# Kernel tuning notes

Measured on AMD Instinct MI355X. Metric: run time of the kernel, lower is better.

Reference implementation:

```python
import jax, jax.numpy as jnp
import numpy as np
from jax import lax

B, T, C_IN, HID, K, HORIZON = 64, 1024, 256, 512, 3, 12
OUT_DIM = HORIZON * 3


def causal_conv(x, w, b, dilation):
    # x: (B, C_in, T), w: (C_out, C_in, K) -> left-padded causal conv == conv+Chomp1d
    pad = (K - 1) * dilation
    y = lax.conv_general_dilated(x, w, window_strides=(1,), padding=[(pad, 0)],
                                 rhs_dilation=(dilation,),
                                 dimension_numbers=('NCH', 'OIH', 'NCH'))
    return y + b[None, :, None]


def setup_inputs() -> dict:
    key = jax.random.key(0)
    ks = jax.random.split(key, 16)
    N = B * T
    x = jax.random.normal(ks[0], (N, C_IN), jnp.float32)
    edge_index = jax.random.randint(ks[1], (2, N), 0, N, dtype=jnp.int64)
    idx = jnp.arange(N, dtype=jnp.int64)
    batch = idx // T          # graph id per node
    node_time = idx % T       # local time per node
    s1 = 1.0 / np.sqrt(C_IN * K)
    s2 = 1.0 / np.sqrt(HID * K)
    sd = 1.0 / np.sqrt(C_IN)
    sf = 1.0 / np.sqrt(HID)
    return {
        'x': x, 'edge_index': edge_index, 'batch': batch, 'node_time': node_time,
        # TemporalBlock 0 (in=C_IN, out=HID, dilation=1)
        'conv1_w0': jax.random.uniform(ks[2], (HID, C_IN, K), jnp.float32, -s1, s1),
        'conv1_b0': jax.random.uniform(ks[3], (HID,), jnp.float32, -s1, s1),
        'conv2_w0': jax.random.uniform(ks[4], (HID, HID, K), jnp.float32, -s2, s2),
        'conv2_b0': jax.random.uniform(ks[5], (HID,), jnp.float32, -s2, s2),
        'down_w0': jax.random.uniform(ks[6], (HID, C_IN, 1), jnp.float32, -sd, sd),
        'down_b0': jax.random.uniform(ks[7], (HID,), jnp.float32, -sd, sd),
        # TemporalBlock 1 (in=HID, out=HID, dilation=2, no downsample)
        'conv1_w1': jax.random.uniform(ks[8], (HID, HID, K), jnp.float32, -s2, s2),
        'conv1_b1': jax.random.uniform(ks[9], (HID,), jnp.float32, -s2, s2),
        'conv2_w1': jax.random.uniform(ks[10], (HID, HID, K), jnp.float32, -s2, s2),
        'conv2_b1': jax.random.uniform(ks[11], (HID,), jnp.float32, -s2, s2),
        # fc
        'fc_w': jax.random.uniform(ks[12], (OUT_DIM, HID), jnp.float32, -sf, sf),
        'fc_b': jax.random.uniform(ks[13], (OUT_DIM,), jnp.float32, -sf, sf),
    }


def reference(x, edge_index, batch, node_time,
              conv1_w0, conv1_b0, conv2_w0, conv2_b0, down_w0, down_b0,
              conv1_w1, conv1_b1, conv2_w1, conv2_b1, fc_w, fc_b):
    # vectorized scatter replacing the per-node Python loop
    x_seq = jnp.zeros((B, T, C_IN), x.dtype).at[batch, node_time].set(x)
    h = x_seq.transpose(0, 2, 1)  # (B, C_IN, T)
    # TemporalBlock 0 (dropout inactive in eval)
    out = jax.nn.relu(causal_conv(h, conv1_w0, conv1_b0, 1))
    out = jax.nn.relu(causal_conv(out, conv2_w0, conv2_b0, 1))
    res = jnp.einsum('bct,oc->bot', h, down_w0[:, :, 0]) + down_b0[None, :, None]
    h = jax.nn.relu(out + res)
    # TemporalBlock 1
    out = jax.nn.relu(causal_conv(h, conv1_w1, conv1_b1, 2))
    out = jax.nn.relu(causal_conv(out, conv2_w1, conv2_b1, 2))
    h = jax.nn.relu(out + h)
    # last timestep -> fc
    return h[:, :, -1] @ fc_w.T + fc_b
```

## Files before the change

### kernel.cpp

```cpp
#include <hip/hip_runtime.h>


#define OUTD 36

template <int CIN, int TS_N, int TP, int TOUT, int S, int D, int OFF, int TAPS,
          int OCT, int CCH, int NCH, bool SRC_X, int TS_BASE, int TS_STEP>
__device__ __forceinline__ void conv_body(int bx, int by,
                                          const float* __restrict__ src,
                                          const float* __restrict__ w,
                                          float* __restrict__ Pout) {
    const int tid = threadIdx.x, lane = tid & 63, wv = tid >> 6;
    const int oc0 = bx * OCT;
    constexpr int OCR = OCT / 4;
    __shared__ float Als[CCH * TAPS * OCT];
    __shared__ float Bls[CCH * 64 * TP];
    float acc[OCR][TOUT];
#pragma unroll
    for (int i = 0; i < OCR; ++i)
#pragma unroll
        for (int t = 0; t < TOUT; ++t) acc[i][t] = 0.f;

    for (int ch = 0; ch < NCH; ++ch) {
        const int c0 = (by * NCH + ch) * CCH;
        if (ch) __syncthreads();
        for (int idx = tid; idx < OCT * CCH * TAPS; idx += 256) {
            int i = idx / (CCH * TAPS), r = idx % (CCH * TAPS);
            int c = r / TAPS, kk = r % TAPS;
            Als[(c * TAPS + kk) * OCT + i] =
                w[(size_t)(oc0 + i) * (CIN * TAPS) + (c0 + c) * TAPS + kk];
        }
        if constexpr (SRC_X) {
            for (int idx = tid; idx < CCH * TS_N * 64; idx += 256) {
                int c = idx % CCH, rb = idx / CCH;
                int b = rb & 63, u = rb >> 6;
                Bls[(c * 64 + b) * TP + u] =
                    src[((size_t)b * 1024 + 1011 + TS_BASE + TS_STEP * u) * 256 +
                        c0 + c];
            }
        } else {
            const float4* gp = (const float4*)(src + (size_t)c0 * 64 * TP);
            float4* lp = (float4*)Bls;
            for (int idx = tid; idx < CCH * 64 * TP / 4; idx += 256)
                lp[idx] = gp[idx];
        }
        __syncthreads();
        constexpr int NLOAD = (TP % 4 == 0) ? TP : TS_N;
        for (int c = 0; c < CCH; ++c) {
            float bv[NLOAD];
            if constexpr (TP % 4 == 0) {
#pragma unroll
                for (int q = 0; q < TP / 4; ++q)
                    *(float4*)&bv[4 * q] =
                        *(const float4*)&Bls[(c * 64 + lane) * TP + 4 * q];
            } else {
#pragma unroll
                for (int u = 0; u < TS_N; ++u)
                    bv[u] = Bls[(c * 64 + lane) * TP + u];
            }
            float av[TAPS][OCR];
#pragma unroll
            for (int kk = 0; kk < TAPS; ++kk)
#pragma unroll
                for (int j = 0; j < OCR; j += 4)
                    *(float4*)&av[kk][j] =
                        *(const float4*)&Als[(c * TAPS + kk) * OCT + wv * OCR + j];
#pragma unroll
            for (int i = 0; i < OCR; ++i)
#pragma unroll
                for (int t = 0; t < TOUT; ++t)
#pragma unroll
                    for (int kk = 0; kk < TAPS; ++kk)
                        acc[i][t] += av[kk][i] * bv[S * t + D * kk + OFF];
        }
    }
#pragma unroll
    for (int i = 0; i < OCR; ++i)
#pragma unroll
        for (int t = 0; t < TOUT; ++t)
            Pout[(((size_t)by * 512 + oc0 + wv * OCR + i) * TOUT + t) * 64 +
                 lane] = acc[i][t];
}

template <int CIN, int TS_N, int TP, int TOUT, int S, int D, int OFF, int TAPS,
          int OCT, int CCH, int NCH, bool SRC_X, int TS_BASE, int TS_STEP>
__global__ __launch_bounds__(256) void k_conv(const float* __restrict__ src,
                                              const float* __restrict__ w,
                                              float* __restrict__ Pout) {
    conv_body<CIN, TS_N, TP, TOUT, S, D, OFF, TAPS, OCT, CCH, NCH, SRC_X,
              TS_BASE, TS_STEP>(blockIdx.x, blockIdx.y, src, w, Pout);
}

__global__ __launch_bounds__(256) void k_l0dn(const float* __restrict__ x,
                                              const float* __restrict__ w1_0,
                                              const float* __restrict__ wd0,
                                              float* __restrict__ P0,
                                              float* __restrict__ PD) {
    if (blockIdx.x < 256) {
        conv_body<256, 13, 13, 11, 1, 1, 0, 3, 16, 16, 2, true, 0, 1>(
            blockIdx.x >> 3, blockIdx.x & 7, x, w1_0, P0);
    } else {
        const int q = blockIdx.x - 256;
        conv_body<256, 5, 5, 5, 1, 0, 0, 1, 32, 16, 2, true, 4, 2>(
            q >> 3, q & 7, x, wd0, PD);
    }
}

template <int KS1, int T, int TPo, int KS2, bool RES>
__global__ __launch_bounds__(256) void k_red(const float* __restrict__ P1,
                                             const float* __restrict__ bias1,
                                             const float* __restrict__ P2,
                                             const float* __restrict__ bias2,
                                             const float* __restrict__ res,
                                             float* __restrict__ outp) {
    const int oc = blockIdx.x, tid = threadIdx.x;
    __shared__ float Sm[64 * TPo];
    if constexpr (TPo > 1) {
        for (int i = tid; i < 64 * TPo; i += 256) Sm[i] = 0.f;
        __syncthreads();
    }
    if (tid < T * 16) {
        const int t = tid / 16, b4 = (tid % 16) * 4;
        float4 s = make_float4(0.f, 0.f, 0.f, 0.f);
#pragma unroll
        for (int p = 0; p < KS1; ++p) {
            float4 u =
                *(const float4*)(P1 + (((size_t)p * 512 + oc) * T + t) * 64 + b4);
            s.x += u.x; s.y += u.y; s.z += u.z; s.w += u.w;
        }
        const float b1 = bias1[oc];
        s.x = fmaxf(s.x + b1, 0.f); s.y = fmaxf(s.y + b1, 0.f);
        s.z = fmaxf(s.z + b1, 0.f); s.w = fmaxf(s.w + b1, 0.f);
        if constexpr (KS2 > 0) {
            float4 s2 = make_float4(0.f, 0.f, 0.f, 0.f);
#pragma unroll
            for (int p = 0; p < KS2; ++p) {
                float4 u =
                    *(const float4*)(P2 + (((size_t)p * 512 + oc) * T + t) * 64 + b4);
                s2.x += u.x; s2.y += u.y; s2.z += u.z; s2.w += u.w;
            }
            const float b2v = bias2[oc];
            s.x = fmaxf(s.x + s2.x + b2v, 0.f);
            s.y = fmaxf(s.y + s2.y + b2v, 0.f);
            s.z = fmaxf(s.z + s2.z + b2v, 0.f);
            s.w = fmaxf(s.w + s2.w + b2v, 0.f);
        }
        if constexpr (RES) {
            s.x = fmaxf(s.x + res[((size_t)oc * 64 + b4 + 0) * 12 + 4], 0.f);
            s.y = fmaxf(s.y + res[((size_t)oc * 64 + b4 + 1) * 12 + 4], 0.f);
            s.z = fmaxf(s.z + res[((size_t)oc * 64 + b4 + 2) * 12 + 4], 0.f);
            s.w = fmaxf(s.w + res[((size_t)oc * 64 + b4 + 3) * 12 + 4], 0.f);
        }
        if constexpr (TPo == 1) {
            *(float4*)(outp + (size_t)oc * 64 + b4) = s;
        } else {
            Sm[(b4 + 0) * TPo + t] = s.x;
            Sm[(b4 + 1) * TPo + t] = s.y;
            Sm[(b4 + 2) * TPo + t] = s.z;
            Sm[(b4 + 3) * TPo + t] = s.w;
        }
    }
    if constexpr (TPo > 1) {
        __syncthreads();
        float4* op = (float4*)(outp + (size_t)oc * 64 * TPo);
        for (int i = tid; i < 64 * TPo / 4; i += 256)
            op[i] = *(const float4*)&Sm[4 * i];
    }
}

__global__ __launch_bounds__(64) void k_fc(const float* __restrict__ H1,
                                           const float* __restrict__ fcw,
                                           const float* __restrict__ fcb,
                                           float* __restrict__ out) {
    const int j = blockIdx.x, lane = threadIdx.x;
    float acc = fcb[j];
#pragma unroll 8
    for (int o = 0; o < 512; ++o) acc += fcw[j * 512 + o] * H1[o * 64 + lane];
    out[lane * OUTD + j] = acc;
}

extern "C" void kernel_launch(void* const* d_in, const int* in_sizes, int n_in,
                              void* d_out, int out_size, void* d_ws, size_t ws_size,
                              hipStream_t stream) {
    const float* x    = (const float*)d_in[0];
    const float* w1_0 = (const float*)d_in[4];
    const float* b1_0 = (const float*)d_in[5];
    const float* w2_0 = (const float*)d_in[6];
    const float* b2_0 = (const float*)d_in[7];
    const float* wd0  = (const float*)d_in[8];
    const float* bd0  = (const float*)d_in[9];
    const float* w1_1 = (const float*)d_in[10];
    const float* b1_1 = (const float*)d_in[11];
    const float* w2_1 = (const float*)d_in[12];
    const float* b2_1 = (const float*)d_in[13];
    const float* fcw  = (const float*)d_in[14];
    const float* fcb  = (const float*)d_in[15];
    float* out = (float*)d_out;

    float* P0  = (float*)d_ws;
    float* B1  = P0 + 8 * 512 * 11 * 64;
    float* P1  = B1 + 512 * 64 * 12;
    float* PD  = P1 + 16 * 512 * 5 * 64;
    float* H0  = PD + 8 * 512 * 5 * 64;
    float* P2  = H0 + 512 * 64 * 12;
    float* B2  = P2 + 16 * 512 * 3 * 64;
    float* P3  = B2 + 512 * 64 * 4;
    float* H1g = P3 + 8 * 512 * 64;

    k_l0dn<<<384, 256, 0, stream>>>(x, w1_0, wd0, P0, PD);
    k_red<8, 11, 12, 0, false><<<512, 256, 0, stream>>>(P0, b1_0, nullptr,
                                                        nullptr, nullptr, B1);
    k_conv<512, 11, 12, 5, 2, 1, 0, 3, 32, 16, 2, false, 0, 0>
        <<<dim3(16, 16), 256, 0, stream>>>(B1, w2_0, P1);
    k_red<16, 5, 12, 8, false><<<512, 256, 0, stream>>>(P1, b2_0, PD, bd0,
                                                        nullptr, H0);
    k_conv<512, 5, 12, 3, 1, 1, 0, 3, 32, 16, 2, false, 0, 0>
        <<<dim3(16, 16), 256, 0, stream>>>(H0, w1_1, P2);
    k_red<16, 3, 4, 0, false><<<512, 256, 0, stream>>>(P2, b1_1, nullptr,
                                                       nullptr, nullptr, B2);
    k_conv<512, 3, 4, 1, 1, 1, 0, 3, 32, 32, 2, false, 0, 0>
        <<<dim3(16, 8), 256, 0, stream>>>(B2, w2_1, P3);
    k_red<8, 1, 1, 0, true><<<512, 256, 0, stream>>>(P3, b2_1, nullptr, nullptr,
                                                     H0, H1g);
    k_fc<<<OUTD, 64, 0, stream>>>(H1g, fcw, fcb, out);
}
```

Baseline: 117.7 us.

## Fuse block-1 reductions into conv and fc kernels, halve split-K partials

Replaces the last five launches (conv, reduce, conv, reduce, fc) with three. The block-1 conv1 now uses fewer split-K partitions (8 instead of 16). A new kernel kD sums those partials, applies bias and ReLU while staging into shared memory, and does the final dilated conv. A new kernel kE folds the conv2 partial reduction, the residual ReLU and the fc layer into one pass. The aim is to cut launch overhead and intermediate global round-trips, at the cost of less parallelism in the fc kernel (36 blocks) and the conv kernel.

```diff
diff --git a/kernel.cpp b/kernel.cpp
--- a/kernel.cpp
+++ b/kernel.cpp
@@ -2,6 +2,22 @@
 
 
 #define OUTD 36
+#define F4(q) (*(const float4*)(q))
+
+__device__ __forceinline__ float relu(float v) { return fmaxf(v, 0.f); }
+__device__ __forceinline__ float4 relu4(float4 v) {
+  v.x = fmaxf(v.x, 0.f); v.y = fmaxf(v.y, 0.f);
+  v.z = fmaxf(v.z, 0.f); v.w = fmaxf(v.w, 0.f);
+  return v;
+}
+__device__ __forceinline__ float4 add4(float4 a, float4 b) {
+  a.x += b.x; a.y += b.y; a.z += b.z; a.w += b.w;
+  return a;
+}
+__device__ __forceinline__ float4 addc4(float4 a, float c) {
+  a.x += c; a.y += c; a.z += c; a.w += c;
+  return a;
+}
 
 template <int CIN, int TS_N, int TP, int TOUT, int S, int D, int OFF, int TAPS,
           int OCT, int CCH, int NCH, bool SRC_X, int TS_BASE, int TS_STEP>
@@ -122,27 +138,16 @@
         const int t = tid / 16, b4 = (tid % 16) * 4;
         float4 s = make_float4(0.f, 0.f, 0.f, 0.f);
 #pragma unroll
-        for (int p = 0; p < KS1; ++p) {
-            float4 u =
-                *(const float4*)(P1 + (((size_t)p * 512 + oc) * T + t) * 64 + b4);
-            s.x += u.x; s.y += u.y; s.z += u.z; s.w += u.w;
-        }
+        for (int p = 0; p < KS1; ++p)
+            s = add4(s, F4(P1 + (((size_t)p * 512 + oc) * T + t) * 64 + b4));
         const float b1 = bias1[oc];
-        s.x = fmaxf(s.x + b1, 0.f); s.y = fmaxf(s.y + b1, 0.f);
-        s.z = fmaxf(s.z + b1, 0.f); s.w = fmaxf(s.w + b1, 0.f);
+        s = relu4(addc4(s, b1));
         if constexpr (KS2 > 0) {
             float4 s2 = make_float4(0.f, 0.f, 0.f, 0.f);
 #pragma unroll
-            for (int p = 0; p < KS2; ++p) {
-                float4 u =
-                    *(const float4*)(P2 + (((size_t)p * 512 + oc) * T + t) * 64 + b4);
-                s2.x += u.x; s2.y += u.y; s2.z += u.z; s2.w += u.w;
-            }
-            const float b2v = bias2[oc];
-            s.x = fmaxf(s.x + s2.x + b2v, 0.f);
-            s.y = fmaxf(s.y + s2.y + b2v, 0.f);
-            s.z = fmaxf(s.z + s2.z + b2v, 0.f);
-            s.w = fmaxf(s.w + s2.w + b2v, 0.f);
+            for (int p = 0; p < KS2; ++p)
+                s2 = add4(s2, F4(P2 + (((size_t)p * 512 + oc) * T + t) * 64 + b4));
+            s = relu4(addc4(add4(s, s2), bias2[oc]));
         }
         if constexpr (RES) {
             s.x = fmaxf(s.x + res[((size_t)oc * 64 + b4 + 0) * 12 + 4], 0.f);
@@ -167,15 +172,75 @@
     }
 }
 
-__global__ __launch_bounds__(64) void k_fc(const float* __restrict__ H1,
-                                           const float* __restrict__ fcw,
-                                           const float* __restrict__ fcb,
-                                           float* __restrict__ out) {
-    const int j = blockIdx.x, lane = threadIdx.x;
-    float acc = fcb[j];
-#pragma unroll 8
-    for (int o = 0; o < 512; ++o) acc += fcw[j * 512 + o] * H1[o * 64 + lane];
-    out[lane * OUTD + j] = acc;
+__global__ __launch_bounds__(256) void kD(const float* __restrict__ P2,
+                                          const float* __restrict__ b1_1,
+                                          const float* __restrict__ w2_1,
+                                          float* __restrict__ P3) {
+  __shared__ float smem[18432];
+  const int tid = threadIdx.x, lane = tid & 63, wv = tid >> 6;
+  const int ocp = blockIdx.x >> 3, ks = blockIdx.x & 7, oc0 = ocp * 32;
+  const int c0 = ks * 64;
+  float* Als = smem;
+  float* Bls = smem + 6144;
+  float acc[8];
+#pragma unroll
+  for (int i = 0; i < 8; ++i) acc[i] = 0.f;
+  for (int idx = tid; idx < 6144; idx += 256) {
+    int i = idx / 192, r = idx % 192, c = r / 3, kk = r % 3;
+    Als[(c * 3 + kk) * 32 + i] = w2_1[(oc0 + i) * 1536 + (c0 + c) * 3 + kk];
+  }
+  for (int idx = tid; idx < 3072; idx += 256) {
+    int c = idx / 48, r = idx % 48, u = r / 16, b4 = (r & 15) * 4;
+    int cc = c0 + c;
+    float4 s = {0.f, 0.f, 0.f, 0.f};
+#pragma unroll
+    for (int p = 0; p < 8; ++p)
+      s = add4(s, F4(&P2[((p * 512 + cc) * 3 + u) * 64 + b4]));
+    *(float4*)&Bls[(c * 3 + u) * 64 + b4] = relu4(addc4(s, b1_1[cc]));
+  }
+  __syncthreads();
+  for (int c = 0; c < 64; ++c) {
+    float bv[3];
+#pragma unroll
+    for (int u = 0; u < 3; ++u) bv[u] = Bls[(c * 3 + u) * 64 + lane];
+    float av[3][8];
+#pragma unroll
+    for (int kk = 0; kk < 3; ++kk) {
+      *(float4*)&av[kk][0] = F4(&Als[(c * 3 + kk) * 32 + wv * 8]);
+      *(float4*)&av[kk][4] = F4(&Als[(c * 3 + kk) * 32 + wv * 8 + 4]);
+    }
+#pragma unroll
+    for (int i = 0; i < 8; ++i)
+#pragma unroll
+      for (int kk = 0; kk < 3; ++kk) acc[i] += av[kk][i] * bv[kk];
+  }
+#pragma unroll
+  for (int i = 0; i < 8; ++i)
+    P3[(ks * 512 + oc0 + wv * 8 + i) * 64 + lane] = acc[i];
+}
+
+__global__ __launch_bounds__(256) void kE(const float* __restrict__ P3,
+                                          const float* __restrict__ b2_1,
+                                          const float* __restrict__ H0,
+                                          const float* __restrict__ fcw,
+                                          const float* __restrict__ fcb,
+                                          float* __restrict__ out) {
+  const int j = blockIdx.x, tid = threadIdx.x;
+  const int lane = tid & 63, wv = tid >> 6;
+  __shared__ float red[4][64];
+  float partial = (wv == 0) ? fcb[j] : 0.f;
+  for (int o = wv * 128; o < wv * 128 + 128; ++o) {
+    float s = 0.f;
+#pragma unroll
+    for (int p = 0; p < 8; ++p) s += P3[(p * 512 + o) * 64 + lane];
+    float h1 = relu(relu(s + b2_1[o]) + H0[((size_t)o * 64 + lane) * 12 + 4]);
+    partial += fcw[j * 512 + o] * h1;
+  }
+  red[wv][lane] = partial;
+  __syncthreads();
+  if (wv == 0)
+    out[lane * OUTD + j] =
+        red[0][lane] + red[1][lane] + red[2][lane] + red[3][lane];
 }
 
 extern "C" void kernel_launch(void* const* d_in, const int* in_sizes, int n_in,
@@ -202,9 +267,7 @@
     float* PD  = P1 + 16 * 512 * 5 * 64;
     float* H0  = PD + 8 * 512 * 5 * 64;
     float* P2  = H0 + 512 * 64 * 12;
-    float* B2  = P2 + 16 * 512 * 3 * 64;
-    float* P3  = B2 + 512 * 64 * 4;
-    float* H1g = P3 + 8 * 512 * 64;
+    float* P3  = P2 + 8 * 512 * 3 * 64;
 
     k_l0dn<<<384, 256, 0, stream>>>(x, w1_0, wd0, P0, PD);
     k_red<8, 11, 12, 0, false><<<512, 256, 0, stream>>>(P0, b1_0, nullptr,
@@ -213,13 +276,8 @@
         <<<dim3(16, 16), 256, 0, stream>>>(B1, w2_0, P1);
     k_red<16, 5, 12, 8, false><<<512, 256, 0, stream>>>(P1, b2_0, PD, bd0,
                                                         nullptr, H0);
-    k_conv<512, 5, 12, 3, 1, 1, 0, 3, 32, 16, 2, false, 0, 0>
-        <<<dim3(16, 16), 256, 0, stream>>>(H0, w1_1, P2);
-    k_red<16, 3, 4, 0, false><<<512, 256, 0, stream>>>(P2, b1_1, nullptr,
-                                                       nullptr, nullptr, B2);
-    k_conv<512, 3, 4, 1, 1, 1, 0, 3, 32, 32, 2, false, 0, 0>
-        <<<dim3(16, 8), 256, 0, stream>>>(B2, w2_1, P3);
-    k_red<8, 1, 1, 0, true><<<512, 256, 0, stream>>>(P3, b2_1, nullptr, nullptr,
-                                                     H0, H1g);
-    k_fc<<<OUTD, 64, 0, stream>>>(H1g, fcw, fcb, out);
-}
+    k_conv<512, 5, 12, 3, 1, 1, 0, 3, 32, 16, 4, false, 0, 0>
+        <<<dim3(16, 8), 256, 0, stream>>>(H0, w1_1, P2);
+    kD<<<128, 256, 0, stream>>>(P2, b1_1, w2_1, P3);
+    kE<<<OUTD, 256, 0, stream>>>(P3, b2_1, H0, fcw, fcb, out);
+}
```

Measured after the change: 151.1 us. 1.28x slower.
